# Kernel optimization log

Hardware: AMD Instinct MI355X
Metric: run time of the kernel (lower is better)

The kernel has to match this reference:

```python
import jax, jax.numpy as jnp
import numpy as np

B, S, H, NH = 2, 2048, 768, 12
HD = H // NH  # 64


def setup_inputs() -> dict:
    key = jax.random.key(0)
    ks = jax.random.split(key, 4)
    scale = 1.0 / np.sqrt(H)
    return {
        "hidden_states": jax.random.normal(ks[0], (B, S, H), dtype=jnp.float32),
        "Wq": jax.random.normal(ks[1], (H, H), dtype=jnp.float32) * scale,
        "bq": jnp.zeros((H,), dtype=jnp.float32),
        "Wk": jax.random.normal(ks[2], (H, H), dtype=jnp.float32) * scale,
        "bk": jnp.zeros((H,), dtype=jnp.float32),
        "Wv": jax.random.normal(ks[3], (H, H), dtype=jnp.float32) * scale,
        "bv": jnp.zeros((H,), dtype=jnp.float32),
    }


def _split_heads(x):
    # [B,S,H] -> [B,NH,S,HD]  (transpose_for_scores)
    b, s, _ = x.shape
    return x.reshape(b, s, NH, HD).transpose(0, 2, 1, 3)


def reference(hidden_states, Wq, bq, Wk, bk, Wv, bv):
    q = _split_heads(hidden_states @ Wq + bq)  # [B,NH,S,HD]
    k = _split_heads(hidden_states @ Wk + bk)
    v = _split_heads(hidden_states @ Wv + bv)
    # delegated attn_fn(q,k,v): scaled-dot-product softmax attention
    scores = jnp.einsum("bhqd,bhkd->bhqk", q, k) / jnp.sqrt(jnp.asarray(HD, q.dtype))
    probs = jax.nn.softmax(scores, axis=-1)
    ctx = jnp.einsum("bhqk,bhkd->bhqd", probs, v)  # [B,NH,S,HD]
    # merge heads back: permute(0,2,1,3) then view to [B,S,H]
    out = ctx.transpose(0, 2, 1, 3).reshape(B, S, NH * HD)
    return out
```

## Files before the change

kernel.cpp:

```cpp
#include <hip/hip_runtime.h>
#include <stdint.h>

typedef __bf16 bf16_t;
typedef __bf16 bf16x8 __attribute__((ext_vector_type(8)));
typedef float f32x4 __attribute__((ext_vector_type(4)));
typedef float f32x16 __attribute__((ext_vector_type(16)));

#define DEV __device__ __forceinline__

DEV void gload_lds16(const void* g, void* lds) {
  __builtin_amdgcn_global_load_lds(
      (const __attribute__((address_space(1))) uint32_t*)g,
      (__attribute__((address_space(3))) uint32_t*)lds, 16, 0, 0);
}

DEV float fexp2(float x) {
#if __has_builtin(__builtin_amdgcn_exp2f)
  return __builtin_amdgcn_exp2f(x);
#else
  return exp2f(x);
#endif
}

DEV uint32_t pk_bf16(float a, float b) {
  uint32_t lo = (uint32_t)__builtin_bit_cast(uint16_t, (bf16_t)a);
  uint32_t hi = (uint32_t)__builtin_bit_cast(uint16_t, (bf16_t)b);
  return lo | (hi << 16);
}

__global__ __launch_bounds__(256) void cvt_hs(const float* __restrict__ x,
                                              bf16_t* __restrict__ y) {
  int i = blockIdx.x * 256 + threadIdx.x;
  float4 v = ((const float4*)x)[i];
  ((uint2*)y)[i] = make_uint2(pk_bf16(v.x, v.y), pk_bf16(v.z, v.w));
}

__global__ __launch_bounds__(256) void cvt_w(const float* __restrict__ Wq,
                                             const float* __restrict__ Wk,
                                             const float* __restrict__ Wv,
                                             bf16_t* __restrict__ WT) {
  __shared__ float T[32][36];
  const int bx = blockIdx.x;
  const int by = blockIdx.y;
  const int p = bx / 24;
  const float* W = (p == 0) ? Wq : ((p == 1) ? Wk : Wv);
  const int n0 = bx * 32, nn0 = n0 - p * 768, k0 = by * 32;
  const int t = threadIdx.x;
  {
    int r = t >> 3, c4 = (t & 7) * 4;
    float4 v = *(const float4*)&W[(size_t)(k0 + r) * 768 + nn0 + c4];
    T[r][c4 + 0] = v.x; T[r][c4 + 1] = v.y; T[r][c4 + 2] = v.z; T[r][c4 + 3] = v.w;
  }
  __syncthreads();
  {
    int nr = t >> 3, kc = (t & 7) * 4;
    uint32_t lo = pk_bf16(T[kc + 0][nr], T[kc + 1][nr]);
    uint32_t hi = pk_bf16(T[kc + 2][nr], T[kc + 3][nr]);
    *(uint2*)&WT[(size_t)(n0 + nr) * 768 + k0 + kc] = make_uint2(lo, hi);
  }
}

__global__ __launch_bounds__(256) void gemm_qkv(
    const bf16_t* __restrict__ A, const bf16_t* __restrict__ Wt,
    const float* __restrict__ bq, const float* __restrict__ bk,
    const float* __restrict__ bv, bf16_t* __restrict__ Qo,
    bf16_t* __restrict__ Ko, bf16_t* __restrict__ VTo) {
  __shared__ __align__(16) char smem[34816];
  bf16_t* As = (bf16_t*)smem;
  bf16_t* Bs = As + 128 * 64;
  bf16_t* Cs = (bf16_t*)smem;
  const int bx = blockIdx.x;
  const int by = blockIdx.y;
  const int m0 = by * 128, n0 = bx * 128;
  const int tid = threadIdx.x, w = tid >> 6, lane = tid & 63;
  const int mw = (w & 1) * 64, nw = (w >> 1) * 64;
  const int quad = lane >> 4, col = lane & 15;

  f32x4 acc[4][4];
  for (int i = 0; i < 4; i++)
    for (int j = 0; j < 4; j++) acc[i][j] = (f32x4){0.f, 0.f, 0.f, 0.f};

  const int srow = w * 32 + (lane >> 3);
  const int scol = (lane & 7) * 8;
  const bf16_t* ag = A + (size_t)(m0 + srow) * 768 + scol;
  const bf16_t* bg = Wt + (size_t)(n0 + srow) * 768 + scol;

  for (int kk = 0; kk < 12; ++kk) {
    const int k0 = kk * 64;
    __syncthreads();
#pragma unroll
    for (int i = 0; i < 4; i++) {
      gload_lds16(ag + (size_t)i * 8 * 768 + k0, As + (w * 32 + i * 8) * 64);
      gload_lds16(bg + (size_t)i * 8 * 768 + k0, Bs + (w * 32 + i * 8) * 64);
    }
    __syncthreads();
#pragma unroll
    for (int ks = 0; ks < 2; ++ks) {
      bf16x8 af[4], bf[4];
#pragma unroll
      for (int mt = 0; mt < 4; ++mt)
        af[mt] = *(const bf16x8*)&As[(mw + mt * 16 + col) * 64 + ks * 32 + quad * 8];
#pragma unroll
      for (int nt = 0; nt < 4; ++nt)
        bf[nt] = *(const bf16x8*)&Bs[(nw + nt * 16 + col) * 64 + ks * 32 + quad * 8];
#pragma unroll
      for (int mt = 0; mt < 4; ++mt)
#pragma unroll
        for (int nt = 0; nt < 4; ++nt)
          acc[mt][nt] = __builtin_amdgcn_mfma_f32_16x16x32_bf16(
              af[mt], bf[nt], acc[mt][nt], 0, 0, 0);
    }
  }

  const int p = bx / 6;
  const float* bp = (p == 0) ? bq : ((p == 1) ? bk : bv);
  const float kscale = (p == 1) ? 0.18033688011112042f : 1.0f;
  const int bb0 = m0 >> 11, s0 = m0 & 2047;
  __syncthreads();
  if (p < 2) {
#pragma unroll
    for (int nt = 0; nt < 4; nt++) {
      int n = nw + nt * 16 + col;
      float bias = bp[n0 + n - p * 768];
#pragma unroll
      for (int mt = 0; mt < 4; mt++)
#pragma unroll
        for (int r = 0; r < 4; r++) {
          int m = mw + mt * 16 + quad * 4 + r;
          Cs[m * 136 + n] = (bf16_t)((acc[mt][nt][r] + bias) * kscale);
        }
    }
    __syncthreads();
    bf16_t* dst = (p == 0) ? Qo : Ko;
#pragma unroll
    for (int i = 0; i < 8; i++) {
      int idx = i * 256 + tid;
      int m = idx >> 4, c = idx & 15;
      bf16x8 v = *(const bf16x8*)&Cs[m * 136 + c * 8];
      int nn = n0 - p * 768 + c * 8;
      int hq = nn >> 6, hd = nn & 63;
      *(bf16x8*)&dst[(size_t)((bb0 * 12 + hq) * 2048 + s0 + m) * 64 + hd] = v;
    }
  } else {
#pragma unroll
    for (int nt = 0; nt < 4; nt++) {
      int n = nw + nt * 16 + col;
      float bias = bp[n0 + n - 1536];
#pragma unroll
      for (int mt = 0; mt < 4; mt++)
#pragma unroll
        for (int r = 0; r < 4; r++) {
          int m = mw + mt * 16 + quad * 4 + r;
          Cs[n * 136 + m] = (bf16_t)(acc[mt][nt][r] + bias);
        }
    }
    __syncthreads();
#pragma unroll
    for (int i = 0; i < 8; i++) {
      int idx = i * 256 + tid;
      int n = idx >> 4, c = idx & 15;
      bf16x8 v = *(const bf16x8*)&Cs[n * 136 + c * 8];
      int nn = n0 - 1536 + n;
      int hq = nn >> 6, hd = nn & 63;
      *(bf16x8*)&VTo[((size_t)(bb0 * 12 + hq) * 64 + hd) * 2048 + s0 + c * 8] = v;
    }
  }
}

__global__ __launch_bounds__(128) void attn(const bf16_t* __restrict__ Q,
                                            const bf16_t* __restrict__ K,
                                            const bf16_t* __restrict__ VT,
                                            float* __restrict__ out) {
  __shared__ bf16_t Kl[2][64 * 64];
  __shared__ bf16_t Vl[2][64 * 64];
  const int qt = blockIdx.x;
  const int bh = blockIdx.y;
  const int b = bh / 12, head = bh % 12;
  const int tid = threadIdx.x, wv = tid >> 6, lane = tid & 63;
  const int lq = lane & 31, half = lane >> 5;
  const int q0 = qt * 64 + wv * 32;

  bf16x8 qf[4];
#pragma unroll
  for (int ks = 0; ks < 4; ++ks)
    qf[ks] = *(const bf16x8*)&Q[(size_t)(bh * 2048 + q0 + lq) * 64 + ks * 16 + half * 8];

  f32x16 oacc[2];
  for (int i = 0; i < 16; i++) { oacc[0][i] = 0.f; oacc[1][i] = 0.f; }
  float l_own = 0.f;

  const bf16_t* gK = K + (size_t)bh * 2048 * 64;
  const bf16_t* gV = VT + (size_t)bh * 64 * 2048;
  const int srow = lane >> 3, scc = lane & 7;

  auto stage = [&](int kb, int bb) {
    if (wv == 0) {
#pragma unroll
      for (int i = 0; i < 8; i++) {
        int row = i * 8 + srow, cg = scc ^ (row & 7);
        gload_lds16(gK + (size_t)(kb * 64 + row) * 64 + cg * 8, &Kl[bb][i * 512]);
      }
    } else {
#pragma unroll
      for (int i = 0; i < 8; i++) {
        int row = i * 8 + srow, cg = scc ^ (row & 7);
        gload_lds16(gV + (size_t)row * 2048 + kb * 64 + cg * 8, &Vl[bb][i * 512]);
      }
    }
  };

  stage(0, 0);
  __syncthreads();

  for (int kb = 0; kb < 32; ++kb) {
    const int bb = kb & 1;
    if (kb < 31) stage(kb + 1, bb ^ 1);

    f32x16 sacc[2];
    for (int i = 0; i < 16; i++) { sacc[0][i] = 0.f; sacc[1][i] = 0.f; }
#pragma unroll
    for (int t = 0; t < 2; t++) {
      const int row = t * 32 + lq;
#pragma unroll
      for (int ks = 0; ks < 4; ++ks) {
        bf16x8 kf = *(const bf16x8*)&Kl[bb][row * 64 + (((2 * ks + half) ^ (row & 7)) * 8)];
        sacc[t] = __builtin_amdgcn_mfma_f32_32x32x16_bf16(kf, qf[ks], sacc[t], 0, 0, 0);
      }
    }

#pragma unroll
    for (int t = 0; t < 2; t++)
#pragma unroll
      for (int r = 0; r < 16; r++) sacc[t][r] = fexp2(sacc[t][r]);
#pragma unroll
    for (int t = 0; t < 2; t++)
#pragma unroll
      for (int r = 0; r < 16; r++) l_own += sacc[t][r];

    uint32_t pk[2][4][2];
#pragma unroll
    for (int t = 0; t < 2; t++)
#pragma unroll
      for (int g = 0; g < 4; g++) {
        pk[t][g][0] = pk_bf16(sacc[t][4 * g + 0], sacc[t][4 * g + 1]);
        pk[t][g][1] = pk_bf16(sacc[t][4 * g + 2], sacc[t][4 * g + 3]);
      }

    bf16x8 pfrag[4];
#pragma unroll
    for (int t = 0; t < 2; t++)
#pragma unroll
      for (int e = 0; e < 2; e++) {
        uint32_t s0 = half ? pk[t][2 * e][0] : pk[t][2 * e + 1][0];
        uint32_t s1 = half ? pk[t][2 * e][1] : pk[t][2 * e + 1][1];
        uint32_t r0 = __shfl_xor(s0, 32);
        uint32_t r1 = __shfl_xor(s1, 32);
        uint32_t o0 = half ? pk[t][2 * e + 1][0] : pk[t][2 * e][0];
        uint32_t o1 = half ? pk[t][2 * e + 1][1] : pk[t][2 * e][1];
        union { uint32_t u[4]; bf16x8 v; } F;
        F.u[0] = half ? r0 : o0;
        F.u[1] = half ? r1 : o1;
        F.u[2] = half ? o0 : r0;
        F.u[3] = half ? o1 : r1;
        pfrag[2 * t + e] = F.v;
      }

#pragma unroll
    for (int c = 0; c < 4; c++) {
#pragma unroll
      for (int dt = 0; dt < 2; dt++) {
        const int vr = dt * 32 + lq;
        bf16x8 vf = *(const bf16x8*)&Vl[bb][vr * 64 + (((2 * c + half) ^ (vr & 7)) * 8)];
        oacc[dt] = __builtin_amdgcn_mfma_f32_32x32x16_bf16(vf, pfrag[c], oacc[dt], 0, 0, 0);
      }
    }
    __syncthreads();
  }

  float l_tot = l_own + __shfl_xor(l_own, 32);
  float inv = 1.0f / l_tot;
  __syncthreads();
  float* Of = (float*)&Kl[wv][0];
#pragma unroll
  for (int dt = 0; dt < 2; dt++)
#pragma unroll
    for (int r = 0; r < 16; r++) {
      int d = dt * 32 + (r & 3) + 8 * (r >> 2) + 4 * half;
      int g = d >> 2, wd = d & 3;
      Of[lq * 64 + ((g ^ (lq & 15)) * 4) + wd] = oacc[dt][r] * inv;
    }
  float* ob = out + ((size_t)b * 2048 + q0) * 768 + head * 64;
#pragma unroll
  for (int i = 0; i < 8; i++) {
    int idx = i * 64 + lane;
    int q = idx >> 4, c = idx & 15;
    f32x4 v = *(f32x4*)&Of[q * 64 + ((c ^ (q & 15)) * 4)];
    *(f32x4*)&ob[(size_t)q * 768 + c * 4] = v;
  }
}

extern "C" void kernel_launch(void* const* d_in, const int* in_sizes, int n_in,
                              void* d_out, int out_size, void* d_ws, size_t ws_size,
                              hipStream_t stream) {
  const float* hs = (const float*)d_in[0];
  const float* Wq = (const float*)d_in[1];
  const float* bq = (const float*)d_in[2];
  const float* Wk = (const float*)d_in[3];
  const float* bk = (const float*)d_in[4];
  const float* Wv = (const float*)d_in[5];
  const float* bv = (const float*)d_in[6];
  float* out = (float*)d_out;

  char* w = (char*)d_ws;
  bf16_t* hsb = (bf16_t*)w; w += (size_t)4096 * 768 * 2;
  bf16_t* wtb = (bf16_t*)w; w += (size_t)2304 * 768 * 2;
  bf16_t* Qb  = (bf16_t*)w; w += (size_t)24 * 2048 * 64 * 2;
  bf16_t* Kb  = (bf16_t*)w; w += (size_t)24 * 2048 * 64 * 2;
  bf16_t* VTb = (bf16_t*)w;

  hipLaunchKernelGGL(cvt_hs, dim3(3072), dim3(256), 0, stream, hs, hsb);
  hipLaunchKernelGGL(cvt_w, dim3(72, 24), dim3(256), 0, stream, Wq, Wk, Wv, wtb);
  hipLaunchKernelGGL(gemm_qkv, dim3(18, 32), dim3(256), 0, stream, hsb, wtb, bq,
                     bk, bv, Qb, Kb, VTb);
  hipLaunchKernelGGL(attn, dim3(32, 24), dim3(128), 0, stream, Qb, Kb, VTb, out);
}
```

Measured before the change: 170.8 us.

## Triple-buffer attention K/V loads, remap blocks, use permlane32 swap and setprio

```diff
diff --git a/kernel.cpp b/kernel.cpp
--- a/kernel.cpp
+++ b/kernel.cpp
@@ -5,6 +5,7 @@
 typedef __bf16 bf16x8 __attribute__((ext_vector_type(8)));
 typedef float f32x4 __attribute__((ext_vector_type(4)));
 typedef float f32x16 __attribute__((ext_vector_type(16)));
+typedef unsigned int u32x2 __attribute__((ext_vector_type(2)));
 
 #define DEV __device__ __forceinline__
 
@@ -171,10 +172,12 @@
                                             const bf16_t* __restrict__ K,
                                             const bf16_t* __restrict__ VT,
                                             float* __restrict__ out) {
-  __shared__ bf16_t Kl[2][64 * 64];
-  __shared__ bf16_t Vl[2][64 * 64];
-  const int qt = blockIdx.x;
-  const int bh = blockIdx.y;
+  __shared__ bf16_t Kl[3][64 * 64];
+  __shared__ bf16_t Vl[3][64 * 64];
+  const int id = blockIdx.x;
+  const int r = id >> 3;
+  const int bh = (id & 7) * 3 + (r >> 5);
+  const int qt = r & 31;
   const int b = bh / 12, head = bh % 12;
   const int tid = threadIdx.x, wv = tid >> 6, lane = tid & 63;
   const int lq = lane & 31, half = lane >> 5;
@@ -187,37 +190,40 @@
 
   f32x16 oacc[2];
   for (int i = 0; i < 16; i++) { oacc[0][i] = 0.f; oacc[1][i] = 0.f; }
-  float l_own = 0.f;
+  float l0 = 0.f, l1 = 0.f, l2 = 0.f, l3 = 0.f;
 
   const bf16_t* gK = K + (size_t)bh * 2048 * 64;
   const bf16_t* gV = VT + (size_t)bh * 64 * 2048;
   const int srow = lane >> 3, scc = lane & 7;
-
-  auto stage = [&](int kb, int bb) {
+  const int cg = scc ^ srow;
+  const bf16_t* gKb = gK + srow * 64 + cg * 8;
+  const bf16_t* gVb = gV + srow * 2048 + cg * 8;
+
+  auto stage = [&](int kb, int buf) {
     if (wv == 0) {
 #pragma unroll
-      for (int i = 0; i < 8; i++) {
-        int row = i * 8 + srow, cg = scc ^ (row & 7);
-        gload_lds16(gK + (size_t)(kb * 64 + row) * 64 + cg * 8, &Kl[bb][i * 512]);
-      }
+      for (int i = 0; i < 8; i++)
+        gload_lds16(gKb + kb * 4096 + i * 512, &Kl[buf][i * 512]);
     } else {
 #pragma unroll
-      for (int i = 0; i < 8; i++) {
-        int row = i * 8 + srow, cg = scc ^ (row & 7);
-        gload_lds16(gV + (size_t)row * 2048 + kb * 64 + cg * 8, &Vl[bb][i * 512]);
-      }
+      for (int i = 0; i < 8; i++)
+        gload_lds16(gVb + i * 16384 + kb * 64, &Vl[buf][i * 512]);
     }
   };
 
   stage(0, 0);
-  __syncthreads();
-
+  stage(1, 1);
+  asm volatile("s_waitcnt vmcnt(8)" ::: "memory");
+  __builtin_amdgcn_s_barrier();
+  asm volatile("" ::: "memory");
+
+  int bb = 0, rb = 2;
   for (int kb = 0; kb < 32; ++kb) {
-    const int bb = kb & 1;
-    if (kb < 31) stage(kb + 1, bb ^ 1);
+    if (kb < 30) stage(kb + 2, rb);
 
     f32x16 sacc[2];
     for (int i = 0; i < 16; i++) { sacc[0][i] = 0.f; sacc[1][i] = 0.f; }
+    __builtin_amdgcn_s_setprio(1);
 #pragma unroll
     for (int t = 0; t < 2; t++) {
       const int row = t * 32 + lq;
@@ -227,44 +233,55 @@
         sacc[t] = __builtin_amdgcn_mfma_f32_32x32x16_bf16(kf, qf[ks], sacc[t], 0, 0, 0);
       }
     }
+    __builtin_amdgcn_s_setprio(0);
 
 #pragma unroll
     for (int t = 0; t < 2; t++)
 #pragma unroll
-      for (int r = 0; r < 16; r++) sacc[t][r] = fexp2(sacc[t][r]);
+      for (int rr = 0; rr < 16; rr++) sacc[t][rr] = fexp2(sacc[t][rr]);
+#pragma unroll
+    for (int rr = 0; rr < 16; rr += 4) {
+      l0 += sacc[0][rr + 0] + sacc[1][rr + 0];
+      l1 += sacc[0][rr + 1] + sacc[1][rr + 1];
+      l2 += sacc[0][rr + 2] + sacc[1][rr + 2];
+      l3 += sacc[0][rr + 3] + sacc[1][rr + 3];
+    }
+
+    uint32_t pkq[2][4][2];
 #pragma unroll
     for (int t = 0; t < 2; t++)
 #pragma unroll
-      for (int r = 0; r < 16; r++) l_own += sacc[t][r];
-
-    uint32_t pk[2][4][2];
+      for (int g = 0; g < 4; g++) {
+        pkq[t][g][0] = pk_bf16(sacc[t][4 * g + 0], sacc[t][4 * g + 1]);
+        pkq[t][g][1] = pk_bf16(sacc[t][4 * g + 2], sacc[t][4 * g + 3]);
+      }
+
+    bf16x8 pfrag[4];
 #pragma unroll
     for (int t = 0; t < 2; t++)
 #pragma unroll
-      for (int g = 0; g < 4; g++) {
-        pk[t][g][0] = pk_bf16(sacc[t][4 * g + 0], sacc[t][4 * g + 1]);
-        pk[t][g][1] = pk_bf16(sacc[t][4 * g + 2], sacc[t][4 * g + 3]);
-      }
-
-    bf16x8 pfrag[4];
-#pragma unroll
-    for (int t = 0; t < 2; t++)
-#pragma unroll
       for (int e = 0; e < 2; e++) {
-        uint32_t s0 = half ? pk[t][2 * e][0] : pk[t][2 * e + 1][0];
-        uint32_t s1 = half ? pk[t][2 * e][1] : pk[t][2 * e + 1][1];
-        uint32_t r0 = __shfl_xor(s0, 32);
-        uint32_t r1 = __shfl_xor(s1, 32);
-        uint32_t o0 = half ? pk[t][2 * e + 1][0] : pk[t][2 * e][0];
-        uint32_t o1 = half ? pk[t][2 * e + 1][1] : pk[t][2 * e][1];
         union { uint32_t u[4]; bf16x8 v; } F;
-        F.u[0] = half ? r0 : o0;
-        F.u[1] = half ? r1 : o1;
-        F.u[2] = half ? o0 : r0;
-        F.u[3] = half ? o1 : r1;
+#pragma unroll
+        for (int wd = 0; wd < 2; wd++) {
+#if __has_builtin(__builtin_amdgcn_permlane32_swap)
+          u32x2 sw = __builtin_amdgcn_permlane32_swap(pkq[t][2 * e][wd],
+                                                      pkq[t][2 * e + 1][wd],
+                                                      false, false);
+          F.u[wd] = sw.x;
+          F.u[2 + wd] = sw.y;
+#else
+          uint32_t s = half ? pkq[t][2 * e][wd] : pkq[t][2 * e + 1][wd];
+          uint32_t rx = __shfl_xor(s, 32);
+          uint32_t ow = half ? pkq[t][2 * e + 1][wd] : pkq[t][2 * e][wd];
+          F.u[wd] = half ? rx : ow;
+          F.u[2 + wd] = half ? ow : rx;
+#endif
+        }
         pfrag[2 * t + e] = F.v;
       }
 
+    __builtin_amdgcn_s_setprio(1);
 #pragma unroll
     for (int c = 0; c < 4; c++) {
 #pragma unroll
@@ -274,9 +291,22 @@
         oacc[dt] = __builtin_amdgcn_mfma_f32_32x32x16_bf16(vf, pfrag[c], oacc[dt], 0, 0, 0);
       }
     }
-    __syncthreads();
-  }
-
+    __builtin_amdgcn_s_setprio(0);
+
+    if (kb < 30) {
+      asm volatile("s_waitcnt vmcnt(8)" ::: "memory");
+    } else if (kb == 30) {
+      asm volatile("s_waitcnt vmcnt(0)" ::: "memory");
+    }
+    if (kb < 31) {
+      __builtin_amdgcn_s_barrier();
+      asm volatile("" ::: "memory");
+    }
+    bb = (bb == 2) ? 0 : bb + 1;
+    rb = (rb == 2) ? 0 : rb + 1;
+  }
+
+  float l_own = (l0 + l1) + (l2 + l3);
   float l_tot = l_own + __shfl_xor(l_own, 32);
   float inv = 1.0f / l_tot;
   __syncthreads();
@@ -284,10 +314,10 @@
 #pragma unroll
   for (int dt = 0; dt < 2; dt++)
 #pragma unroll
-    for (int r = 0; r < 16; r++) {
-      int d = dt * 32 + (r & 3) + 8 * (r >> 2) + 4 * half;
+    for (int rr = 0; rr < 16; rr++) {
+      int d = dt * 32 + (rr & 3) + 8 * (rr >> 2) + 4 * half;
       int g = d >> 2, wd = d & 3;
-      Of[lq * 64 + ((g ^ (lq & 15)) * 4) + wd] = oacc[dt][r] * inv;
+      Of[lq * 64 + ((g ^ (lq & 15)) * 4) + wd] = oacc[dt][rr] * inv;
     }
   float* ob = out + ((size_t)b * 2048 + q0) * 768 + head * 64;
 #pragma unroll
@@ -322,5 +352,5 @@
   hipLaunchKernelGGL(cvt_w, dim3(72, 24), dim3(256), 0, stream, Wq, Wk, Wv, wtb);
   hipLaunchKernelGGL(gemm_qkv, dim3(18, 32), dim3(256), 0, stream, hsb, wtb, bq,
                      bk, bv, Qb, Kb, VTb);
-  hipLaunchKernelGGL(attn, dim3(32, 24), dim3(128), 0, stream, Qb, Kb, VTb, out);
-}
+  hipLaunchKernelGGL(attn, dim3(768), dim3(128), 0, stream, Qb, Kb, VTb, out);
+}
```

Measured after the change: 173.9 us. About the same (+1.8%).
